# Performance work log

Measured on AMD Instinct MI355X. Metric: run time of the kernel, lower is better.

Reference implementation:

```python
import jax, jax.numpy as jnp
import numpy as np

TOP_K = 2


def setup_inputs() -> dict:
    key = jax.random.key(0)
    k1, k2, k3, k4, k5 = jax.random.split(key, 5)
    T, H, I, E = 1024, 1024, 2816, 8
    return {
        "hidden_states": jax.random.normal(k1, (T, H), dtype=jnp.float32),
        "router_logits": jax.random.normal(k2, (T, E), dtype=jnp.float32),
        "w1": jax.random.normal(k3, (E, I, H), dtype=jnp.float32) * 0.02,
        "w3": jax.random.normal(k4, (E, I, H), dtype=jnp.float32) * 0.02,
        "w2": jax.random.normal(k5, (E, H, I), dtype=jnp.float32) * 0.02,
    }


def _gate_weights(router_logits):
    # top-k softmax with renormalization (Mixtral-style routing)
    probs = jax.nn.softmax(router_logits, axis=-1)          # [T, E]
    vals, idx = jax.lax.top_k(probs, TOP_K)                  # [T, K]
    vals = vals / jnp.sum(vals, axis=-1, keepdims=True)
    E = router_logits.shape[-1]
    # dense per-expert gate [T, E]: scatter top-k weights via one-hot
    onehot = jax.nn.one_hot(idx, E, dtype=vals.dtype)        # [T, K, E]
    return jnp.einsum("tk,tke->te", vals, onehot)


def reference(hidden_states, router_logits, w1, w3, w2):
    x = hidden_states.reshape(-1, hidden_states.shape[-1])   # [T, H]
    gate = _gate_weights(router_logits)                      # [T, E]
    # GatedMLP per expert: silu(x @ w1^T) * (x @ w3^T) @ w2^T
    h1 = jnp.einsum("th,eih->tei", x, w1)                    # [T, E, I]
    h3 = jnp.einsum("th,eih->tei", x, w3)
    act = jax.nn.silu(h1) * h3                               # [T, E, I]
    y = jnp.einsum("tei,ehi->teh", act, w2)                  # [T, E, H]
    out = jnp.einsum("teh,te->th", y, gate)                  # weighted combine
    return out
```

## Files before the change

kernel.cpp:

```cpp
#include <hip/hip_runtime.h>
#include <stdint.h>

#define T_TOK 1024
#define H_DIM 1024
#define I_DIM 2816
#define E_NUM 8
#define KSPLIT 2
#define K2_STEPS (I_DIM / 64 / KSPLIT)
#define MAXROWS 3072

typedef __attribute__((ext_vector_type(8))) short bf16x8;
typedef __attribute__((ext_vector_type(4))) float f32x4;

struct Meta { int counts[E_NUM]; int tiles[E_NUM]; int offs[E_NUM]; };

__device__ __forceinline__ unsigned short f2b(float f) {
    unsigned u = __float_as_uint(f);
    u += 0x7fffu + ((u >> 16) & 1u);
    return (unsigned short)(u >> 16);
}

__device__ __forceinline__ uint4 pack8(const float4 a, const float4 b) {
    union { unsigned short us[8]; uint4 v; } u;
    u.us[0] = f2b(a.x); u.us[1] = f2b(a.y); u.us[2] = f2b(a.z); u.us[3] = f2b(a.w);
    u.us[4] = f2b(b.x); u.us[5] = f2b(b.y); u.us[6] = f2b(b.z); u.us[7] = f2b(b.w);
    return u.v;
}

#define SYNC_RAW() do { asm volatile("s_waitcnt lgkmcnt(0)" ::: "memory"); __builtin_amdgcn_s_barrier(); } while (0)

__global__ void route_kernel(const float* __restrict__ logits,
                             int* __restrict__ tok,
                             int4* __restrict__ comb,
                             Meta* __restrict__ meta) {
    __shared__ int cnt[E_NUM];
    __shared__ int soffs[E_NUM];
    const int tid = threadIdx.x;
    if (tid < E_NUM) cnt[tid] = 0;
    for (int j = tid; j < E_NUM * T_TOK; j += 1024) tok[j] = 0;
    __syncthreads();

    float p[E_NUM];
    const float* lrow = logits + tid * E_NUM;
    float m = -1e30f;
    #pragma unroll
    for (int e = 0; e < E_NUM; ++e) { p[e] = lrow[e]; m = fmaxf(m, p[e]); }
    #pragma unroll
    for (int e = 0; e < E_NUM; ++e) p[e] = __expf(p[e] - m);
    int e0 = 0; float v0 = p[0];
    #pragma unroll
    for (int e = 1; e < E_NUM; ++e) if (p[e] > v0) { v0 = p[e]; e0 = e; }
    int e1 = -1; float v1 = -1.f;
    #pragma unroll
    for (int e = 0; e < E_NUM; ++e) if (e != e0 && p[e] > v1) { v1 = p[e]; e1 = e; }
    const float inv = 1.f / (v0 + v1);
    const float g0 = v0 * inv, g1 = v1 * inv;

    const int p0 = atomicAdd(&cnt[e0], 1);
    const int p1 = atomicAdd(&cnt[e1], 1);
    tok[e0 * T_TOK + p0] = tid;
    tok[e1 * T_TOK + p1] = tid;
    __syncthreads();
    if (tid == 0) {
        int off = 0;
        for (int e = 0; e < E_NUM; ++e) {
            const int c = cnt[e];
            const int t = (c + 127) >> 7;
            meta->counts[e] = c; meta->tiles[e] = t; meta->offs[e] = off;
            soffs[e] = off;
            off += t * 128;
        }
    }
    __syncthreads();
    comb[tid] = make_int4(soffs[e0] + p0, soffs[e1] + p1,
                          __float_as_int(g0), __float_as_int(g1));
}

__global__ void cvt_x_kernel(const float* __restrict__ x, unsigned short* __restrict__ xb) {
    const int i = blockIdx.x * blockDim.x + threadIdx.x;
    const float4 v = ((const float4*)x)[i];
    ushort4 o; o.x = f2b(v.x); o.y = f2b(v.y); o.z = f2b(v.z); o.w = f2b(v.w);
    ((ushort4*)xb)[i] = o;
}

__launch_bounds__(512, 4)
__global__ void gemm1_kernel(const unsigned short* __restrict__ xb,
                             const float* __restrict__ w1,
                             const float* __restrict__ w3,
                             const int* __restrict__ tok,
                             const Meta* __restrict__ meta,
                             unsigned short* __restrict__ act) {
    const int e = blockIdx.y;
    const int mt = blockIdx.z;
    if (mt >= meta->tiles[e]) return;
    const int it = blockIdx.x;
    const int tid = threadIdx.x;

    __shared__ __align__(16) unsigned short As[2][128 * 64];
    __shared__ __align__(16) unsigned short B1s[2][64 * 64];
    __shared__ __align__(16) unsigned short B3s[2][64 * 64];

    const int srow = tid >> 3, ssub = tid & 7;
    const int t0 = tok[e * T_TOK + mt * 128 + srow];
    const int t1 = tok[e * T_TOK + mt * 128 + 64 + srow];
    const unsigned short* ap0 = xb + (size_t)t0 * H_DIM + ssub * 8;
    const unsigned short* ap1 = xb + (size_t)t1 * H_DIM + ssub * 8;
    const int scol = (ssub * 8) ^ ((srow & 7) << 3);
    const int aoff0 = srow * 64 + scol;
    const int aoff1 = (64 + srow) * 64 + scol;
    const int boff  = srow * 64 + scol;

    const size_t wbase = (size_t)e * I_DIM * H_DIM + (size_t)(it * 64 + srow) * H_DIM + ssub * 8;
    const float* b1p = w1 + wbase;
    const float* b3p = w3 + wbase;

    const int wave = tid >> 6, lane = tid & 63;
    const int quad = lane >> 4, l15 = lane & 15;
    const int mbase = (wave >> 1) * 32;
    const int nbase = (wave & 1) * 32;

    f32x4 acc1[2][2], acc3[2][2];
    #pragma unroll
    for (int m = 0; m < 2; ++m)
        #pragma unroll
        for (int n = 0; n < 2; ++n) {
            acc1[m][n] = (f32x4){0.f, 0.f, 0.f, 0.f};
            acc3[m][n] = (f32x4){0.f, 0.f, 0.f, 0.f};
        }

#define G1_LOAD(S, koff) do { \
        S##_a0  = *(const uint4*)(ap0 + (koff));      S##_a1  = *(const uint4*)(ap1 + (koff)); \
        S##_b1a = *(const float4*)(b1p + (koff));     S##_b1b = *(const float4*)(b1p + (koff) + 4); \
        S##_b3a = *(const float4*)(b3p + (koff));     S##_b3b = *(const float4*)(b3p + (koff) + 4); \
    } while (0)

#define G1_STORE(S, B) do { \
        *(uint4*)&As[B][aoff0] = S##_a0; \
        *(uint4*)&As[B][aoff1] = S##_a1; \
        *(uint4*)&B1s[B][boff] = pack8(S##_b1a, S##_b1b); \
        *(uint4*)&B3s[B][boff] = pack8(S##_b3a, S##_b3b); \
    } while (0)

#define G1_COMPUTE(B) do { \
        bf16x8 afr[2][2], f1[2][2], f3[2][2]; \
        _Pragma("unroll") \
        for (int m = 0; m < 2; ++m) { \
            const int row = mbase + m * 16 + l15; \
            _Pragma("unroll") \
            for (int kk = 0; kk < 2; ++kk) \
                afr[m][kk] = *(const bf16x8*)&As[B][row * 64 + ((kk * 32 + quad * 8) ^ ((row & 7) << 3))]; \
        } \
        _Pragma("unroll") \
        for (int n = 0; n < 2; ++n) { \
            const int row = nbase + n * 16 + l15; \
            _Pragma("unroll") \
            for (int kk = 0; kk < 2; ++kk) { \
                const int off = row * 64 + ((kk * 32 + quad * 8) ^ ((row & 7) << 3)); \
                f1[n][kk] = *(const bf16x8*)&B1s[B][off]; \
                f3[n][kk] = *(const bf16x8*)&B3s[B][off]; \
            } \
        } \
        _Pragma("unroll") \
        for (int m = 0; m < 2; ++m) \
            _Pragma("unroll") \
            for (int n = 0; n < 2; ++n) \
                _Pragma("unroll") \
                for (int kk = 0; kk < 2; ++kk) { \
                    acc1[m][n] = __builtin_amdgcn_mfma_f32_16x16x32_bf16(afr[m][kk], f1[n][kk], acc1[m][n], 0, 0, 0); \
                    acc3[m][n] = __builtin_amdgcn_mfma_f32_16x16x32_bf16(afr[m][kk], f3[n][kk], acc3[m][n], 0, 0, 0); \
                } \
    } while (0)

    uint4 s0_a0, s0_a1; float4 s0_b1a, s0_b1b, s0_b3a, s0_b3b;
    uint4 s1_a0, s1_a1; float4 s1_b1a, s1_b1b, s1_b3a, s1_b3b;

    const int NK = H_DIM / 64;
    G1_LOAD(s0, 0);
    G1_STORE(s0, 0);
    G1_LOAD(s1, 64);
    SYNC_RAW();

    for (int ks = 0; ks < NK; ks += 2) {
        { const int k2 = (ks + 2 < NK) ? (ks + 2) * 64 : 0; G1_LOAD(s0, k2); }
        G1_COMPUTE(0);
        G1_STORE(s1, 1);
        SYNC_RAW();
        { const int k3 = (ks + 3 < NK) ? (ks + 3) * 64 : 0; G1_LOAD(s1, k3); }
        G1_COMPUTE(1);
        G1_STORE(s0, 0);
        SYNC_RAW();
    }
#undef G1_LOAD
#undef G1_STORE
#undef G1_COMPUTE

    const int opad = meta->offs[e];
    #pragma unroll
    for (int m = 0; m < 2; ++m)
        #pragma unroll
        for (int n = 0; n < 2; ++n)
            #pragma unroll
            for (int rr = 0; rr < 4; ++rr) {
                const float v1 = acc1[m][n][rr];
                const float v3 = acc3[m][n][rr];
                const float s = v1 / (1.f + __expf(-v1)) * v3;
                const int row = opad + mt * 128 + mbase + m * 16 + quad * 4 + rr;
                const int col = it * 64 + nbase + n * 16 + l15;
                act[(size_t)row * I_DIM + col] = f2b(s);
            }
}

__launch_bounds__(512, 4)
__global__ void gemm2_kernel(const unsigned short* __restrict__ act,
                             const float* __restrict__ w2,
                             const Meta* __restrict__ meta,
                             float* __restrict__ ybuf) {
    const int e = blockIdx.y;
    const int mt = blockIdx.z >> 1;
    const int kb = blockIdx.z & 1;
    if (mt >= meta->tiles[e]) return;
    const int it = blockIdx.x;
    const int tid = threadIdx.x;
    const int opad = meta->offs[e];

    __shared__ __align__(16) unsigned short As[2][128 * 64];
    __shared__ __align__(16) unsigned short Bs[2][64 * 64];

    const int srow = tid >> 3, ssub = tid & 7;
    const int kbase = kb * (K2_STEPS * 64);
    const unsigned short* ap0 = act + (size_t)(opad + mt * 128 + srow) * I_DIM + kbase + ssub * 8;
    const unsigned short* ap1 = ap0 + (size_t)64 * I_DIM;
    const int scol = (ssub * 8) ^ ((srow & 7) << 3);
    const int aoff0 = srow * 64 + scol;
    const int aoff1 = (64 + srow) * 64 + scol;
    const int boff  = srow * 64 + scol;

    const float* bp = w2 + (size_t)e * H_DIM * I_DIM + (size_t)(it * 64 + srow) * I_DIM + kbase + ssub * 8;

    const int wave = tid >> 6, lane = tid & 63;
    const int quad = lane >> 4, l15 = lane & 15;
    const int mbase = (wave >> 1) * 32;
    const int nbase = (wave & 1) * 32;

    f32x4 acc[2][2];
    #pragma unroll
    for (int m = 0; m < 2; ++m)
        #pragma unroll
        for (int n = 0; n < 2; ++n) acc[m][n] = (f32x4){0.f, 0.f, 0.f, 0.f};

#define G2_LOAD(S, koff) do { \
        S##_a0 = *(const uint4*)(ap0 + (koff));  S##_a1 = *(const uint4*)(ap1 + (koff)); \
        S##_ba = *(const float4*)(bp + (koff));  S##_bb = *(const float4*)(bp + (koff) + 4); \
    } while (0)

#define G2_STORE(S, B) do { \
        *(uint4*)&As[B][aoff0] = S##_a0; \
        *(uint4*)&As[B][aoff1] = S##_a1; \
        *(uint4*)&Bs[B][boff]  = pack8(S##_ba, S##_bb); \
    } while (0)

#define G2_COMPUTE(B) do { \
        bf16x8 afr[2][2], bfr[2][2]; \
        _Pragma("unroll") \
        for (int m = 0; m < 2; ++m) { \
            const int row = mbase + m * 16 + l15; \
            _Pragma("unroll") \
            for (int kk = 0; kk < 2; ++kk) \
                afr[m][kk] = *(const bf16x8*)&As[B][row * 64 + ((kk * 32 + quad * 8) ^ ((row & 7) << 3))]; \
        } \
        _Pragma("unroll") \
        for (int n = 0; n < 2; ++n) { \
            const int row = nbase + n * 16 + l15; \
            _Pragma("unroll") \
            for (int kk = 0; kk < 2; ++kk) \
                bfr[n][kk] = *(const bf16x8*)&Bs[B][row * 64 + ((kk * 32 + quad * 8) ^ ((row & 7) << 3))]; \
        } \
        _Pragma("unroll") \
        for (int m = 0; m < 2; ++m) \
            _Pragma("unroll") \
            for (int n = 0; n < 2; ++n) \
                _Pragma("unroll") \
                for (int kk = 0; kk < 2; ++kk) \
                    acc[m][n] = __builtin_amdgcn_mfma_f32_16x16x32_bf16(afr[m][kk], bfr[n][kk], acc[m][n], 0, 0, 0); \
    } while (0)

    uint4 s0_a0, s0_a1; float4 s0_ba, s0_bb;
    uint4 s1_a0, s1_a1; float4 s1_ba, s1_bb;

    G2_LOAD(s0, 0);
    G2_STORE(s0, 0);
    G2_LOAD(s1, 64);
    SYNC_RAW();

    for (int ks = 0; ks < K2_STEPS; ks += 2) {
        { const int k2 = (ks + 2 < K2_STEPS) ? (ks + 2) * 64 : 0; G2_LOAD(s0, k2); }
        G2_COMPUTE(0);
        G2_STORE(s1, 1);
        SYNC_RAW();
        { const int k3 = (ks + 3 < K2_STEPS) ? (ks + 3) * 64 : 0; G2_LOAD(s1, k3); }
        G2_COMPUTE(1);
        G2_STORE(s0, 0);
        SYNC_RAW();
    }
#undef G2_LOAD
#undef G2_STORE
#undef G2_COMPUTE

    float* yb = ybuf + (size_t)kb * ((size_t)MAXROWS * H_DIM);
    #pragma unroll
    for (int m = 0; m < 2; ++m)
        #pragma unroll
        for (int rr = 0; rr < 4; ++rr) {
            const int grow = opad + mt * 128 + mbase + m * 16 + quad * 4 + rr;
            #pragma unroll
            for (int n = 0; n < 2; ++n) {
                const int col = it * 64 + nbase + n * 16 + l15;
                yb[(size_t)grow * H_DIM + col] = acc[m][n][rr];
            }
        }
}

__global__ void combine_kernel(const float* __restrict__ ybuf,
                               const int4* __restrict__ comb,
                               float* __restrict__ out) {
    const int t = blockIdx.x;
    const int c = threadIdx.x;
    const int4 cb = comb[t];
    const float g0 = __int_as_float(cb.z), g1 = __int_as_float(cb.w);
    const size_t sp = (size_t)MAXROWS * H_DIM;
    const float4 a = ((const float4*)(ybuf + (size_t)cb.x * H_DIM))[c];
    const float4 b = ((const float4*)(ybuf + sp + (size_t)cb.x * H_DIM))[c];
    const float4 d = ((const float4*)(ybuf + (size_t)cb.y * H_DIM))[c];
    const float4 f = ((const float4*)(ybuf + sp + (size_t)cb.y * H_DIM))[c];
    float4 o;
    o.x = g0 * (a.x + b.x) + g1 * (d.x + f.x);
    o.y = g0 * (a.y + b.y) + g1 * (d.y + f.y);
    o.z = g0 * (a.z + b.z) + g1 * (d.z + f.z);
    o.w = g0 * (a.w + b.w) + g1 * (d.w + f.w);
    ((float4*)(out + (size_t)t * H_DIM))[c] = o;
}

extern "C" void kernel_launch(void* const* d_in, const int* in_sizes, int n_in,
                              void* d_out, int out_size, void* d_ws, size_t ws_size,
                              hipStream_t stream) {
    const float* x      = (const float*)d_in[0];
    const float* logits = (const float*)d_in[1];
    const float* w1     = (const float*)d_in[2];
    const float* w3     = (const float*)d_in[3];
    const float* w2     = (const float*)d_in[4];
    float* out = (float*)d_out;

    char* ws = (char*)d_ws;
    int*   tok  = (int*)ws;
    Meta*  meta = (Meta*)(ws + 65536);
    int4*  comb = (int4*)(ws + 69632);
    unsigned short* xb  = (unsigned short*)(ws + 131072);
    unsigned short* act = (unsigned short*)(ws + 2228224);
    float* ybuf = (float*)(ws + 19529728);

    route_kernel<<<1, 1024, 0, stream>>>(logits, tok, comb, meta);
    cvt_x_kernel<<<T_TOK * H_DIM / 4 / 256, 256, 0, stream>>>(x, xb);
    gemm1_kernel<<<dim3(I_DIM / 64, E_NUM, 8), 512, 0, stream>>>(xb, w1, w3, tok, meta, act);
    gemm2_kernel<<<dim3(H_DIM / 64, E_NUM, 8 * KSPLIT), 512, 0, stream>>>(act, w2, meta, ybuf);
    combine_kernel<<<T_TOK, 256, 0, stream>>>(ybuf, comb, out);
}
```

Measured before the change: 332.5 us.

## Rework expert GEMMs with 32x32 MFMA, direct LDS loads and 256-thread blocks

Both expert GEMM kernels are restructured. They drop from 512 to 256 threads per block and switch from 16x16x32 to 32x32x16 bf16 MFMA tiles. The A operand (tokens/activations) is now loaded with global_load_lds directly into a double-buffered LDS tile, while the fp32 weights use a single padded LDS buffer converted from registers. In gemm1 the w1 and w3 products are split across waves and combined through an LDS exchange before the SiLU epilogue. The grid order is swapped so token tiles vary fastest, which should improve weight reuse in cache, at the cost of a single-buffered B tile and extra barriers per k-step.

```diff
diff --git a/kernel.cpp b/kernel.cpp
--- a/kernel.cpp
+++ b/kernel.cpp
@@ -9,8 +9,8 @@
 #define K2_STEPS (I_DIM / 64 / KSPLIT)
 #define MAXROWS 3072
 
-typedef __attribute__((ext_vector_type(8))) short bf16x8;
-typedef __attribute__((ext_vector_type(4))) float f32x4;
+typedef __attribute__((ext_vector_type(8)))  short bf16x8;
+typedef __attribute__((ext_vector_type(16))) float f32x16;
 
 struct Meta { int counts[E_NUM]; int tiles[E_NUM]; int offs[E_NUM]; };
 
@@ -27,7 +27,15 @@
     return u.v;
 }
 
-#define SYNC_RAW() do { asm volatile("s_waitcnt lgkmcnt(0)" ::: "memory"); __builtin_amdgcn_s_barrier(); } while (0)
+#define WAIT_ALL() asm volatile("s_waitcnt vmcnt(0) lgkmcnt(0)" ::: "memory")
+#define BAR() __builtin_amdgcn_s_barrier()
+#define SCHED_FENCE() __builtin_amdgcn_sched_barrier(0)
+
+__device__ __forceinline__ void gload16(const unsigned short* src, unsigned short* ldsdst) {
+    __builtin_amdgcn_global_load_lds(
+        (const __attribute__((address_space(1))) unsigned int*)src,
+        (__attribute__((address_space(3))) unsigned int*)ldsdst, 16, 0, 0);
+}
 
 __global__ void route_kernel(const float* __restrict__ logits,
                              int* __restrict__ tok,
@@ -83,241 +91,248 @@
     ((ushort4*)xb)[i] = o;
 }
 
-__launch_bounds__(512, 4)
+__launch_bounds__(256, 3)
 __global__ void gemm1_kernel(const unsigned short* __restrict__ xb,
                              const float* __restrict__ w1,
                              const float* __restrict__ w3,
                              const int* __restrict__ tok,
                              const Meta* __restrict__ meta,
                              unsigned short* __restrict__ act) {
-    const int e = blockIdx.y;
-    const int mt = blockIdx.z;
+    const int mt = blockIdx.x;
+    const int e  = blockIdx.y;
+    const int it = blockIdx.z;
     if (mt >= meta->tiles[e]) return;
-    const int it = blockIdx.x;
     const int tid = threadIdx.x;
 
     __shared__ __align__(16) unsigned short As[2][128 * 64];
-    __shared__ __align__(16) unsigned short B1s[2][64 * 64];
-    __shared__ __align__(16) unsigned short B3s[2][64 * 64];
-
-    const int srow = tid >> 3, ssub = tid & 7;
-    const int t0 = tok[e * T_TOK + mt * 128 + srow];
-    const int t1 = tok[e * T_TOK + mt * 128 + 64 + srow];
-    const unsigned short* ap0 = xb + (size_t)t0 * H_DIM + ssub * 8;
-    const unsigned short* ap1 = xb + (size_t)t1 * H_DIM + ssub * 8;
-    const int scol = (ssub * 8) ^ ((srow & 7) << 3);
-    const int aoff0 = srow * 64 + scol;
-    const int aoff1 = (64 + srow) * 64 + scol;
-    const int boff  = srow * 64 + scol;
-
-    const size_t wbase = (size_t)e * I_DIM * H_DIM + (size_t)(it * 64 + srow) * H_DIM + ssub * 8;
-    const float* b1p = w1 + wbase;
-    const float* b3p = w3 + wbase;
+    __shared__ __align__(16) unsigned short B1s[64 * 68];
+    __shared__ __align__(16) unsigned short B3s[64 * 68];
 
     const int wave = tid >> 6, lane = tid & 63;
-    const int quad = lane >> 4, l15 = lane & 15;
-    const int mbase = (wave >> 1) * 32;
-    const int nbase = (wave & 1) * 32;
-
-    f32x4 acc1[2][2], acc3[2][2];
-    #pragma unroll
-    for (int m = 0; m < 2; ++m)
+    const int l8 = lane >> 3, c8 = lane & 7;
+
+    const unsigned short* apg[4];
+    #pragma unroll
+    for (int i = 0; i < 4; ++i) {
+        const int R = (wave * 4 + i) * 8 + l8;
+        const int t = tok[e * T_TOK + mt * 128 + R];
+        apg[i] = xb + (size_t)t * H_DIM + (c8 ^ (R & 7)) * 8;
+    }
+
+    const int brow = tid >> 2, bq = tid & 3;
+    const size_t woff = (size_t)e * I_DIM * H_DIM + (size_t)(it * 64 + brow) * H_DIM + bq * 16;
+    const float* b1p = w1 + woff;
+    const float* b3p = w3 + woff;
+    const int bl = brow * 68 + bq * 16;
+
+    const int half = lane >> 5, l31 = lane & 31;
+    const int pos = wave & 1, mat = wave >> 1;
+    const unsigned short* Bw = mat ? B3s : B1s;
+    const int arow0 = (pos * 64 + l31) * 64;
+    const int arow1 = (pos * 64 + 32 + l31) * 64;
+    const int aswz  = l31 & 7;
+    const int bfr0 = (l31) * 68 + half * 8;
+    const int bfr1 = (32 + l31) * 68 + half * 8;
+
+    f32x16 acc00 = {0}, acc01 = {0}, acc10 = {0}, acc11 = {0};
+
+    float4 r0, r1, r2, r3, r4, r5, r6, r7;
+
+#define G1_GLOAD(KS, B) do { \
+        const int koff_ = (KS) * 64; \
+        _Pragma("unroll") \
+        for (int i = 0; i < 4; ++i) \
+            gload16(apg[i] + koff_, &As[B][(wave * 4 + i) * 512 + lane * 8]); \
+    } while (0)
+
+#define G1_LOADB(KS) do { \
+        const int koff_ = (KS) * 64; \
+        r0 = *(const float4*)(b1p + koff_);      r1 = *(const float4*)(b1p + koff_ + 4); \
+        r2 = *(const float4*)(b1p + koff_ + 8);  r3 = *(const float4*)(b1p + koff_ + 12); \
+        r4 = *(const float4*)(b3p + koff_);      r5 = *(const float4*)(b3p + koff_ + 4); \
+        r6 = *(const float4*)(b3p + koff_ + 8);  r7 = *(const float4*)(b3p + koff_ + 12); \
+    } while (0)
+
+#define G1_STOREB() do { \
+        *(uint4*)&B1s[bl]     = pack8(r0, r1); \
+        *(uint4*)&B1s[bl + 8] = pack8(r2, r3); \
+        *(uint4*)&B3s[bl]     = pack8(r4, r5); \
+        *(uint4*)&B3s[bl + 8] = pack8(r6, r7); \
+    } while (0)
+
+#define G1_COMPUTE(B) do { \
+        _Pragma("unroll") \
+        for (int kk = 0; kk < 4; ++kk) { \
+            const int sc = ((kk * 2 + half) ^ aswz) * 8; \
+            bf16x8 a0 = *(const bf16x8*)&As[B][arow0 + sc]; \
+            bf16x8 a1 = *(const bf16x8*)&As[B][arow1 + sc]; \
+            bf16x8 b0 = *(const bf16x8*)&Bw[bfr0 + kk * 16]; \
+            bf16x8 b1 = *(const bf16x8*)&Bw[bfr1 + kk * 16]; \
+            acc00 = __builtin_amdgcn_mfma_f32_32x32x16_bf16(a0, b0, acc00, 0, 0, 0); \
+            acc01 = __builtin_amdgcn_mfma_f32_32x32x16_bf16(a0, b1, acc01, 0, 0, 0); \
+            acc10 = __builtin_amdgcn_mfma_f32_32x32x16_bf16(a1, b0, acc10, 0, 0, 0); \
+            acc11 = __builtin_amdgcn_mfma_f32_32x32x16_bf16(a1, b1, acc11, 0, 0, 0); \
+        } \
+    } while (0)
+
+    G1_GLOAD(0, 0);
+    G1_LOADB(0);
+    G1_STOREB();
+    WAIT_ALL(); BAR();
+
+    const int NK = H_DIM / 64;
+    int cur = 0;
+    for (int ks = 0; ks < NK; ++ks) {
+        const bool pf = (ks + 1 < NK);
+        if (pf) { G1_GLOAD(ks + 1, cur ^ 1); G1_LOADB(ks + 1); }
+        G1_COMPUTE(cur);
+        SCHED_FENCE();
+        BAR();
+        if (pf) G1_STOREB();
+        WAIT_ALL(); BAR();
+        cur ^= 1;
+    }
+#undef G1_GLOAD
+#undef G1_LOADB
+#undef G1_STOREB
+#undef G1_COMPUTE
+
+    float* ex = (float*)&As[0][0];
+    const int opad = meta->offs[e];
+    if (mat == 1) {
         #pragma unroll
-        for (int n = 0; n < 2; ++n) {
-            acc1[m][n] = (f32x4){0.f, 0.f, 0.f, 0.f};
-            acc3[m][n] = (f32x4){0.f, 0.f, 0.f, 0.f};
-        }
-
-#define G1_LOAD(S, koff) do { \
-        S##_a0  = *(const uint4*)(ap0 + (koff));      S##_a1  = *(const uint4*)(ap1 + (koff)); \
-        S##_b1a = *(const float4*)(b1p + (koff));     S##_b1b = *(const float4*)(b1p + (koff) + 4); \
-        S##_b3a = *(const float4*)(b3p + (koff));     S##_b3b = *(const float4*)(b3p + (koff) + 4); \
-    } while (0)
-
-#define G1_STORE(S, B) do { \
-        *(uint4*)&As[B][aoff0] = S##_a0; \
-        *(uint4*)&As[B][aoff1] = S##_a1; \
-        *(uint4*)&B1s[B][boff] = pack8(S##_b1a, S##_b1b); \
-        *(uint4*)&B3s[B][boff] = pack8(S##_b3a, S##_b3b); \
-    } while (0)
-
-#define G1_COMPUTE(B) do { \
-        bf16x8 afr[2][2], f1[2][2], f3[2][2]; \
-        _Pragma("unroll") \
-        for (int m = 0; m < 2; ++m) { \
-            const int row = mbase + m * 16 + l15; \
-            _Pragma("unroll") \
-            for (int kk = 0; kk < 2; ++kk) \
-                afr[m][kk] = *(const bf16x8*)&As[B][row * 64 + ((kk * 32 + quad * 8) ^ ((row & 7) << 3))]; \
-        } \
-        _Pragma("unroll") \
-        for (int n = 0; n < 2; ++n) { \
-            const int row = nbase + n * 16 + l15; \
-            _Pragma("unroll") \
-            for (int kk = 0; kk < 2; ++kk) { \
-                const int off = row * 64 + ((kk * 32 + quad * 8) ^ ((row & 7) << 3)); \
-                f1[n][kk] = *(const bf16x8*)&B1s[B][off]; \
-                f3[n][kk] = *(const bf16x8*)&B3s[B][off]; \
-            } \
-        } \
-        _Pragma("unroll") \
-        for (int m = 0; m < 2; ++m) \
-            _Pragma("unroll") \
-            for (int n = 0; n < 2; ++n) \
-                _Pragma("unroll") \
-                for (int kk = 0; kk < 2; ++kk) { \
-                    acc1[m][n] = __builtin_amdgcn_mfma_f32_16x16x32_bf16(afr[m][kk], f1[n][kk], acc1[m][n], 0, 0, 0); \
-                    acc3[m][n] = __builtin_amdgcn_mfma_f32_16x16x32_bf16(afr[m][kk], f3[n][kk], acc3[m][n], 0, 0, 0); \
-                } \
-    } while (0)
-
-    uint4 s0_a0, s0_a1; float4 s0_b1a, s0_b1b, s0_b3a, s0_b3b;
-    uint4 s1_a0, s1_a1; float4 s1_b1a, s1_b1b, s1_b3a, s1_b3b;
-
-    const int NK = H_DIM / 64;
-    G1_LOAD(s0, 0);
-    G1_STORE(s0, 0);
-    G1_LOAD(s1, 64);
-    SYNC_RAW();
-
-    for (int ks = 0; ks < NK; ks += 2) {
-        { const int k2 = (ks + 2 < NK) ? (ks + 2) * 64 : 0; G1_LOAD(s0, k2); }
-        G1_COMPUTE(0);
-        G1_STORE(s1, 1);
-        SYNC_RAW();
-        { const int k3 = (ks + 3 < NK) ? (ks + 3) * 64 : 0; G1_LOAD(s1, k3); }
-        G1_COMPUTE(1);
-        G1_STORE(s0, 0);
-        SYNC_RAW();
-    }
-#undef G1_LOAD
-#undef G1_STORE
-#undef G1_COMPUTE
-
-    const int opad = meta->offs[e];
-    #pragma unroll
-    for (int m = 0; m < 2; ++m)
+        for (int mi = 0; mi < 2; ++mi)
+            #pragma unroll
+            for (int ni = 0; ni < 2; ++ni) {
+                const f32x16 a = mi == 0 ? (ni == 0 ? acc00 : acc01) : (ni == 0 ? acc10 : acc11);
+                #pragma unroll
+                for (int r = 0; r < 16; ++r) {
+                    const int frow = pos * 64 + mi * 32 + (r & 3) + 8 * (r >> 2) + 4 * half;
+                    ex[frow * 64 + ni * 32 + l31] = a[r];
+                }
+            }
+    }
+    __syncthreads();
+    if (mat == 0) {
         #pragma unroll
-        for (int n = 0; n < 2; ++n)
+        for (int mi = 0; mi < 2; ++mi)
             #pragma unroll
-            for (int rr = 0; rr < 4; ++rr) {
-                const float v1 = acc1[m][n][rr];
-                const float v3 = acc3[m][n][rr];
-                const float s = v1 / (1.f + __expf(-v1)) * v3;
-                const int row = opad + mt * 128 + mbase + m * 16 + quad * 4 + rr;
-                const int col = it * 64 + nbase + n * 16 + l15;
-                act[(size_t)row * I_DIM + col] = f2b(s);
+            for (int ni = 0; ni < 2; ++ni) {
+                const f32x16 a = mi == 0 ? (ni == 0 ? acc00 : acc01) : (ni == 0 ? acc10 : acc11);
+                #pragma unroll
+                for (int r = 0; r < 16; ++r) {
+                    const int frow = pos * 64 + mi * 32 + (r & 3) + 8 * (r >> 2) + 4 * half;
+                    const float v1 = a[r];
+                    const float v3 = ex[frow * 64 + ni * 32 + l31];
+                    const float s = v1 / (1.f + __expf(-v1)) * v3;
+                    act[(size_t)(opad + mt * 128 + frow) * I_DIM + it * 64 + ni * 32 + l31] = f2b(s);
+                }
             }
-}
-
-__launch_bounds__(512, 4)
+    }
+}
+
+__launch_bounds__(256, 3)
 __global__ void gemm2_kernel(const unsigned short* __restrict__ act,
                              const float* __restrict__ w2,
                              const Meta* __restrict__ meta,
                              float* __restrict__ ybuf) {
-    const int e = blockIdx.y;
-    const int mt = blockIdx.z >> 1;
-    const int kb = blockIdx.z & 1;
+    const int mt = blockIdx.x & 7;
+    const int kb = blockIdx.x >> 3;
+    const int e  = blockIdx.y;
+    const int it = blockIdx.z;
     if (mt >= meta->tiles[e]) return;
-    const int it = blockIdx.x;
     const int tid = threadIdx.x;
     const int opad = meta->offs[e];
+    const int kbase = kb * (K2_STEPS * 64);
 
     __shared__ __align__(16) unsigned short As[2][128 * 64];
-    __shared__ __align__(16) unsigned short Bs[2][64 * 64];
-
-    const int srow = tid >> 3, ssub = tid & 7;
-    const int kbase = kb * (K2_STEPS * 64);
-    const unsigned short* ap0 = act + (size_t)(opad + mt * 128 + srow) * I_DIM + kbase + ssub * 8;
-    const unsigned short* ap1 = ap0 + (size_t)64 * I_DIM;
-    const int scol = (ssub * 8) ^ ((srow & 7) << 3);
-    const int aoff0 = srow * 64 + scol;
-    const int aoff1 = (64 + srow) * 64 + scol;
-    const int boff  = srow * 64 + scol;
-
-    const float* bp = w2 + (size_t)e * H_DIM * I_DIM + (size_t)(it * 64 + srow) * I_DIM + kbase + ssub * 8;
+    __shared__ __align__(16) unsigned short Bs[64 * 68];
 
     const int wave = tid >> 6, lane = tid & 63;
-    const int quad = lane >> 4, l15 = lane & 15;
-    const int mbase = (wave >> 1) * 32;
-    const int nbase = (wave & 1) * 32;
-
-    f32x4 acc[2][2];
-    #pragma unroll
-    for (int m = 0; m < 2; ++m)
+    const int l8 = lane >> 3, c8 = lane & 7;
+
+    const unsigned short* apg[4];
+    #pragma unroll
+    for (int i = 0; i < 4; ++i) {
+        const int R = (wave * 4 + i) * 8 + l8;
+        apg[i] = act + (size_t)(opad + mt * 128 + R) * I_DIM + kbase + (c8 ^ (R & 7)) * 8;
+    }
+
+    const int brow = tid >> 2, bq = tid & 3;
+    const float* bp = w2 + (size_t)e * H_DIM * I_DIM + (size_t)(it * 64 + brow) * I_DIM + kbase + bq * 16;
+    const int bl = brow * 68 + bq * 16;
+
+    const int half = lane >> 5, l31 = lane & 31;
+    const int wm = wave >> 1, wn = wave & 1;
+    const int arow0 = (wm * 64 + l31) * 64;
+    const int arow1 = (wm * 64 + 32 + l31) * 64;
+    const int aswz  = l31 & 7;
+    const int bfr = (wn * 32 + l31) * 68 + half * 8;
+
+    f32x16 acc0 = {0}, acc1 = {0};
+    float4 r0, r1, r2, r3;
+
+#define G2_GLOAD(KS, B) do { \
+        const int koff_ = (KS) * 64; \
+        _Pragma("unroll") \
+        for (int i = 0; i < 4; ++i) \
+            gload16(apg[i] + koff_, &As[B][(wave * 4 + i) * 512 + lane * 8]); \
+    } while (0)
+
+#define G2_LOADB(KS) do { \
+        const int koff_ = (KS) * 64; \
+        r0 = *(const float4*)(bp + koff_);      r1 = *(const float4*)(bp + koff_ + 4); \
+        r2 = *(const float4*)(bp + koff_ + 8);  r3 = *(const float4*)(bp + koff_ + 12); \
+    } while (0)
+
+#define G2_STOREB() do { \
+        *(uint4*)&Bs[bl]     = pack8(r0, r1); \
+        *(uint4*)&Bs[bl + 8] = pack8(r2, r3); \
+    } while (0)
+
+#define G2_COMPUTE(B) do { \
+        _Pragma("unroll") \
+        for (int kk = 0; kk < 4; ++kk) { \
+            const int sc = ((kk * 2 + half) ^ aswz) * 8; \
+            bf16x8 a0 = *(const bf16x8*)&As[B][arow0 + sc]; \
+            bf16x8 a1 = *(const bf16x8*)&As[B][arow1 + sc]; \
+            bf16x8 b0 = *(const bf16x8*)&Bs[bfr + kk * 16]; \
+            acc0 = __builtin_amdgcn_mfma_f32_32x32x16_bf16(a0, b0, acc0, 0, 0, 0); \
+            acc1 = __builtin_amdgcn_mfma_f32_32x32x16_bf16(a1, b0, acc1, 0, 0, 0); \
+        } \
+    } while (0)
+
+    G2_GLOAD(0, 0);
+    G2_LOADB(0);
+    G2_STOREB();
+    WAIT_ALL(); BAR();
+
+    int cur = 0;
+    for (int ks = 0; ks < K2_STEPS; ++ks) {
+        const bool pf = (ks + 1 < K2_STEPS);
+        if (pf) { G2_GLOAD(ks + 1, cur ^ 1); G2_LOADB(ks + 1); }
+        G2_COMPUTE(cur);
+        SCHED_FENCE();
+        BAR();
+        if (pf) G2_STOREB();
+        WAIT_ALL(); BAR();
+        cur ^= 1;
+    }
+#undef G2_GLOAD
+#undef G2_LOADB
+#undef G2_STOREB
+#undef G2_COMPUTE
+
+    float* yb = ybuf + (size_t)kb * ((size_t)MAXROWS * H_DIM);
+    #pragma unroll
+    for (int mi = 0; mi < 2; ++mi) {
+        const f32x16 a = mi == 0 ? acc0 : acc1;
         #pragma unroll
-        for (int n = 0; n < 2; ++n) acc[m][n] = (f32x4){0.f, 0.f, 0.f, 0.f};
-
-#define G2_LOAD(S, koff) do { \
-        S##_a0 = *(const uint4*)(ap0 + (koff));  S##_a1 = *(const uint4*)(ap1 + (koff)); \
-        S##_ba = *(const float4*)(bp + (koff));  S##_bb = *(const float4*)(bp + (koff) + 4); \
-    } while (0)
-
-#define G2_STORE(S, B) do { \
-        *(uint4*)&As[B][aoff0] = S##_a0; \
-        *(uint4*)&As[B][aoff1] = S##_a1; \
-        *(uint4*)&Bs[B][boff]  = pack8(S##_ba, S##_bb); \
-    } while (0)
-
-#define G2_COMPUTE(B) do { \
-        bf16x8 afr[2][2], bfr[2][2]; \
-        _Pragma("unroll") \
-        for (int m = 0; m < 2; ++m) { \
-            const int row = mbase + m * 16 + l15; \
-            _Pragma("unroll") \
-            for (int kk = 0; kk < 2; ++kk) \
-                afr[m][kk] = *(const bf16x8*)&As[B][row * 64 + ((kk * 32 + quad * 8) ^ ((row & 7) << 3))]; \
-        } \
-        _Pragma("unroll") \
-        for (int n = 0; n < 2; ++n) { \
-            const int row = nbase + n * 16 + l15; \
-            _Pragma("unroll") \
-            for (int kk = 0; kk < 2; ++kk) \
-                bfr[n][kk] = *(const bf16x8*)&Bs[B][row * 64 + ((kk * 32 + quad * 8) ^ ((row & 7) << 3))]; \
-        } \
-        _Pragma("unroll") \
-        for (int m = 0; m < 2; ++m) \
-            _Pragma("unroll") \
-            for (int n = 0; n < 2; ++n) \
-                _Pragma("unroll") \
-                for (int kk = 0; kk < 2; ++kk) \
-                    acc[m][n] = __builtin_amdgcn_mfma_f32_16x16x32_bf16(afr[m][kk], bfr[n][kk], acc[m][n], 0, 0, 0); \
-    } while (0)
-
-    uint4 s0_a0, s0_a1; float4 s0_ba, s0_bb;
-    uint4 s1_a0, s1_a1; float4 s1_ba, s1_bb;
-
-    G2_LOAD(s0, 0);
-    G2_STORE(s0, 0);
-    G2_LOAD(s1, 64);
-    SYNC_RAW();
-
-    for (int ks = 0; ks < K2_STEPS; ks += 2) {
-        { const int k2 = (ks + 2 < K2_STEPS) ? (ks + 2) * 64 : 0; G2_LOAD(s0, k2); }
-        G2_COMPUTE(0);
-        G2_STORE(s1, 1);
-        SYNC_RAW();
-        { const int k3 = (ks + 3 < K2_STEPS) ? (ks + 3) * 64 : 0; G2_LOAD(s1, k3); }
-        G2_COMPUTE(1);
-        G2_STORE(s0, 0);
-        SYNC_RAW();
-    }
-#undef G2_LOAD
-#undef G2_STORE
-#undef G2_COMPUTE
-
-    float* yb = ybuf + (size_t)kb * ((size_t)MAXROWS * H_DIM);
-    #pragma unroll
-    for (int m = 0; m < 2; ++m)
-        #pragma unroll
-        for (int rr = 0; rr < 4; ++rr) {
-            const int grow = opad + mt * 128 + mbase + m * 16 + quad * 4 + rr;
-            #pragma unroll
-            for (int n = 0; n < 2; ++n) {
-                const int col = it * 64 + nbase + n * 16 + l15;
-                yb[(size_t)grow * H_DIM + col] = acc[m][n][rr];
-            }
+        for (int r = 0; r < 16; ++r) {
+            const int frow = wm * 64 + mi * 32 + (r & 3) + 8 * (r >> 2) + 4 * half;
+            yb[(size_t)(opad + mt * 128 + frow) * H_DIM + it * 64 + wn * 32 + l31] = a[r];
         }
+    }
 }
 
 __global__ void combine_kernel(const float* __restrict__ ybuf,
@@ -360,7 +375,7 @@
 
     route_kernel<<<1, 1024, 0, stream>>>(logits, tok, comb, meta);
     cvt_x_kernel<<<T_TOK * H_DIM / 4 / 256, 256, 0, stream>>>(x, xb);
-    gemm1_kernel<<<dim3(I_DIM / 64, E_NUM, 8), 512, 0, stream>>>(xb, w1, w3, tok, meta, act);
-    gemm2_kernel<<<dim3(H_DIM / 64, E_NUM, 8 * KSPLIT), 512, 0, stream>>>(act, w2, meta, ybuf);
+    gemm1_kernel<<<dim3(8, E_NUM, I_DIM / 64), 256, 0, stream>>>(xb, w1, w3, tok, meta, act);
+    gemm2_kernel<<<dim3(8 * KSPLIT, E_NUM, H_DIM / 64), 256, 0, stream>>>(act, w2, meta, ybuf);
     combine_kernel<<<T_TOK, 256, 0, stream>>>(ybuf, comb, out);
 }
```

Result: slower. 632.3 us (+90.2%).
